# Performance work log

Hardware: AMD Instinct MI355X
Metric: run time of the kernel (lower is better)

## Reference

```python
import jax, jax.numpy as jnp
import numpy as np

BLANK_IDX = -1  # resolves to V-1
BATCH_FIRST = False
IS_PROBS = False


def setup_inputs() -> dict:
    key = jax.random.key(0)
    k1, k2 = jax.random.split(key)
    T, N, V = 2048, 32, 1024
    logits = jax.random.normal(k1, (T, N, V), dtype=jnp.float32)
    in_lens = jax.random.randint(k2, (N,), 1, T + 1).astype(jnp.int64)
    return {"logits": logits, "in_lens": in_lens}


def reference(logits, in_lens):
    # logits: (T, N, V) since batch_first=False
    V = logits.shape[2]
    blank = (BLANK_IDX + V) % V  # = V - 1
    logp = jax.nn.log_softmax(logits, axis=2)
    x = jnp.transpose(logp, (1, 0, 2))  # (N, T, V)
    max_ = jnp.max(x, axis=2)            # (N, T)
    argmax = jnp.argmax(x, axis=2)       # (N, T)
    N, T = argmax.shape

    keep = argmax != blank
    dedup = jnp.concatenate(
        [keep[:, :1], keep[:, 1:] & (argmax[:, 1:] != argmax[:, :-1])], axis=1
    )
    in_len_mask = jnp.arange(T)[None, :] < in_lens[:, None]  # (N, T)
    keep = dedup & in_len_mask
    max_ = jnp.where(in_len_mask, max_, 0.0)

    out_lens = keep.sum(axis=1)  # (N,)
    # stream compaction: position of each kept token within its row
    pos = jnp.cumsum(keep, axis=1) - 1               # (N, T)
    safe_pos = jnp.where(keep, pos, T)               # out-of-bounds -> dropped
    rows = jnp.broadcast_to(jnp.arange(N)[:, None], (N, T))
    # torch masked_scatter_ semantics: overwrite first out_lens[n] slots,
    # leave remaining entries as original argmax values ("undefined" region)
    paths = argmax.at[rows, safe_pos].set(argmax, mode="drop")

    max_total = max_.sum(axis=1)  # (N,)
    if not BATCH_FIRST:
        paths = paths.T  # (T, N)
    return max_total, paths, out_lens
```

## Files before the change

kernel.cpp:

```cpp
#include <hip/hip_runtime.h>
#include <hip/hip_bf16.h>


#define WAVE 64

template <int CH>
__global__ __launch_bounds__(256) void row_lse_kernel(
    const float* __restrict__ logits,
    float* __restrict__ rmaxT, int* __restrict__ rargT,
    int T, int N, int rows) {
  const int lane = threadIdx.x & (WAVE - 1);
  const int row  = blockIdx.x * (blockDim.x >> 6) + (threadIdx.x >> 6);
  if (row >= rows) return;
  const int V = CH * 256;
  const float* p = logits + (size_t)row * V;

  float m = -3.4e38f;
  int   mi = 0;
  float4 v[CH];
#pragma unroll
  for (int c = 0; c < CH; ++c) {
    const int idx = c * 256 + lane * 4;
    v[c] = *(const float4*)(p + idx);
    if (v[c].x > m) { m = v[c].x; mi = idx; }
    if (v[c].y > m) { m = v[c].y; mi = idx + 1; }
    if (v[c].z > m) { m = v[c].z; mi = idx + 2; }
    if (v[c].w > m) { m = v[c].w; mi = idx + 3; }
  }
#pragma unroll
  for (int off = 32; off; off >>= 1) {
    const float om = __shfl_down(m, off);
    const int   oi = __shfl_down(mi, off);
    if (om > m || (om == m && oi < mi)) { m = om; mi = oi; }
  }
  m = __shfl(m, 0);

  float s = 0.f;
#pragma unroll
  for (int c = 0; c < CH; ++c)
    s += __expf(v[c].x - m) + __expf(v[c].y - m) +
         __expf(v[c].z - m) + __expf(v[c].w - m);
#pragma unroll
  for (int off = 32; off; off >>= 1) s += __shfl_down(s, off);

  if (lane == 0) {
    const int t = row / N, n = row % N;
    rmaxT[(size_t)n * T + t] = -__logf(s);
    rargT[(size_t)n * T + t] = mi;
  }
}

__global__ __launch_bounds__(256) void row_lse_generic(
    const float* __restrict__ logits,
    float* __restrict__ rmaxT, int* __restrict__ rargT,
    int T, int N, int V, int rows) {
  const int lane = threadIdx.x & (WAVE - 1);
  const int row  = blockIdx.x * (blockDim.x >> 6) + (threadIdx.x >> 6);
  if (row >= rows) return;
  const float* p = logits + (size_t)row * V;

  float m = -3.4e38f; int mi = 0;
  for (int i = lane; i < V; i += WAVE) {
    const float x = p[i];
    if (x > m) { m = x; mi = i; }
  }
  for (int off = 32; off; off >>= 1) {
    const float om = __shfl_down(m, off);
    const int   oi = __shfl_down(mi, off);
    if (om > m || (om == m && oi < mi)) { m = om; mi = oi; }
  }
  m = __shfl(m, 0);
  float s = 0.f;
  for (int i = lane; i < V; i += WAVE) s += __expf(p[i] - m);
  for (int off = 32; off; off >>= 1) s += __shfl_down(s, off);
  if (lane == 0) {
    const int t = row / N, n = row % N;
    rmaxT[(size_t)n * T + t] = -__logf(s);
    rargT[(size_t)n * T + t] = mi;
  }
}

#define CB 256
__global__ __launch_bounds__(CB) void ctc_compact_kernel(
    const float* __restrict__ rmaxT, const int* __restrict__ rargT,
    const int* __restrict__ in_lens, float* __restrict__ out,
    int T, int N, int V) {
  const int n = blockIdx.x;
  const int tid = threadIdx.x;
  const int L = in_lens[n];
  const int blank = V - 1;
  const int items = (T + CB - 1) / CB;
  const int t0 = tid * items;

  float* out_total = out;
  float* out_paths = out + N;
  float* out_lens  = out + N + (size_t)T * N;

  const float* rm = rmaxT + (size_t)n * T;
  const int*   ra = rargT + (size_t)n * T;

  int   cnt = 0;
  float sum = 0.f;
  for (int i = 0; i < items; ++i) {
    const int t = t0 + i;
    if (t >= T) break;
    const int a = ra[t];
    bool keep = (t < L) && (a != blank);
    if (keep && t > 0) keep = (a != ra[t - 1]);
    cnt += keep ? 1 : 0;
    if (t < L) sum += rm[t];
    out_paths[(size_t)t * N + n] = (float)a;
  }

  __shared__ int   s_cnt[CB];
  __shared__ float s_sum[CB];
  s_cnt[tid] = cnt;
  s_sum[tid] = sum;
  __syncthreads();
  for (int off = 1; off < CB; off <<= 1) {
    const int   c  = (tid >= off) ? s_cnt[tid - off] : 0;
    const float sv = (tid >= off) ? s_sum[tid - off] : 0.f;
    __syncthreads();
    s_cnt[tid] += c;
    s_sum[tid] += sv;
    __syncthreads();
  }
  const int prefix = s_cnt[tid] - cnt;
  if (tid == 0) {
    out_total[n] = s_sum[CB - 1];
    out_lens[n]  = (float)s_cnt[CB - 1];
  }
  __syncthreads();

  int pos = prefix;
  for (int i = 0; i < items; ++i) {
    const int t = t0 + i;
    if (t >= T) break;
    const int a = ra[t];
    bool keep = (t < L) && (a != blank);
    if (keep && t > 0) keep = (a != ra[t - 1]);
    if (keep) {
      out_paths[(size_t)pos * N + n] = (float)a;
      ++pos;
    }
  }
}

extern "C" void kernel_launch(void* const* d_in, const int* in_sizes, int n_in,
                              void* d_out, int out_size, void* d_ws, size_t ws_size,
                              hipStream_t stream) {
  const float* logits = (const float*)d_in[0];
  const int* in_lens  = (const int*)d_in[1];
  float* out = (float*)d_out;

  const int N = in_sizes[1];
  const int T = (out_size - 2 * N) / N;
  const long long total = in_sizes[0];
  const int V = (int)(total / ((long long)T * N));
  const int rows = T * N;

  float* rmaxT = (float*)d_ws;
  int*   rargT = (int*)((char*)d_ws + (size_t)rows * sizeof(float));

  const int wavesPerBlock = 4;
  const int grid1 = (rows + wavesPerBlock - 1) / wavesPerBlock;

  if (V == 1024) {
    row_lse_kernel<4><<<grid1, 256, 0, stream>>>(logits, rmaxT, rargT, T, N, rows);
  } else if (V == 512) {
    row_lse_kernel<2><<<grid1, 256, 0, stream>>>(logits, rmaxT, rargT, T, N, rows);
  } else if (V == 2048) {
    row_lse_kernel<8><<<grid1, 256, 0, stream>>>(logits, rmaxT, rargT, T, N, rows);
  } else {
    row_lse_generic<<<grid1, 256, 0, stream>>>(logits, rmaxT, rargT, T, N, V, rows);
  }

  ctc_compact_kernel<<<N, CB, 0, stream>>>(rmaxT, rargT, in_lens, out, T, N, V);
}
```

Baseline: 359.4 us.

## Write raw argmax paths from LSE kernel, use nontemporal loads, carry prev argmax

The row-reduction kernel now writes the uncompacted argmax value for each (t,n) row directly into the output paths buffer, coalesced through shared memory. This removes the strided scatter of the full path array from the per-sequence compaction kernel, which now only overwrites the kept prefix. Logit loads become nontemporal to avoid polluting the cache on a streaming read. The compaction loops carry the previous argmax in a register instead of reloading it. One barrier is dropped, and the cross-kernel ordering between the two writes to the paths buffer is relied on for correctness.

```diff
diff --git a/kernel.cpp b/kernel.cpp
--- a/kernel.cpp
+++ b/kernel.cpp
@@ -3,25 +3,30 @@
 
 
 #define WAVE 64
+
+typedef float nvec4 __attribute__((ext_vector_type(4)));
 
 template <int CH>
 __global__ __launch_bounds__(256) void row_lse_kernel(
     const float* __restrict__ logits,
     float* __restrict__ rmaxT, int* __restrict__ rargT,
+    float* __restrict__ out_paths,
     int T, int N, int rows) {
   const int lane = threadIdx.x & (WAVE - 1);
-  const int row  = blockIdx.x * (blockDim.x >> 6) + (threadIdx.x >> 6);
-  if (row >= rows) return;
+  const int w    = threadIdx.x >> 6;
+  const int row  = blockIdx.x * 4 + w;
+  const bool active = row < rows;
   const int V = CH * 256;
-  const float* p = logits + (size_t)row * V;
+  const float* p = logits + (size_t)(active ? row : 0) * V;
+  const nvec4* p4 = (const nvec4*)p;
 
   float m = -3.4e38f;
   int   mi = 0;
-  float4 v[CH];
+  nvec4 v[CH];
 #pragma unroll
   for (int c = 0; c < CH; ++c) {
+    v[c] = __builtin_nontemporal_load(p4 + c * 64 + lane);
     const int idx = c * 256 + lane * 4;
-    v[c] = *(const float4*)(p + idx);
     if (v[c].x > m) { m = v[c].x; mi = idx; }
     if (v[c].y > m) { m = v[c].y; mi = idx + 1; }
     if (v[c].z > m) { m = v[c].z; mi = idx + 2; }
@@ -43,21 +48,30 @@
 #pragma unroll
   for (int off = 32; off; off >>= 1) s += __shfl_down(s, off);
 
-  if (lane == 0) {
+  __shared__ float s_path[4];
+  if (lane == 0 && active) {
     const int t = row / N, n = row % N;
     rmaxT[(size_t)n * T + t] = -__logf(s);
     rargT[(size_t)n * T + t] = mi;
+    s_path[w] = (float)mi;
+  }
+  __syncthreads();
+  if (threadIdx.x < 4) {
+    const int r = blockIdx.x * 4 + threadIdx.x;
+    if (r < rows) out_paths[r] = s_path[threadIdx.x];
   }
 }
 
 __global__ __launch_bounds__(256) void row_lse_generic(
     const float* __restrict__ logits,
     float* __restrict__ rmaxT, int* __restrict__ rargT,
+    float* __restrict__ out_paths,
     int T, int N, int V, int rows) {
   const int lane = threadIdx.x & (WAVE - 1);
-  const int row  = blockIdx.x * (blockDim.x >> 6) + (threadIdx.x >> 6);
-  if (row >= rows) return;
-  const float* p = logits + (size_t)row * V;
+  const int w    = threadIdx.x >> 6;
+  const int row  = blockIdx.x * 4 + w;
+  const bool active = row < rows;
+  const float* p = logits + (size_t)(active ? row : 0) * V;
 
   float m = -3.4e38f; int mi = 0;
   for (int i = lane; i < V; i += WAVE) {
@@ -73,10 +87,18 @@
   float s = 0.f;
   for (int i = lane; i < V; i += WAVE) s += __expf(p[i] - m);
   for (int off = 32; off; off >>= 1) s += __shfl_down(s, off);
-  if (lane == 0) {
+
+  __shared__ float s_path[4];
+  if (lane == 0 && active) {
     const int t = row / N, n = row % N;
     rmaxT[(size_t)n * T + t] = -__logf(s);
     rargT[(size_t)n * T + t] = mi;
+    s_path[w] = (float)mi;
+  }
+  __syncthreads();
+  if (threadIdx.x < 4) {
+    const int r = blockIdx.x * 4 + threadIdx.x;
+    if (r < rows) out_paths[r] = s_path[threadIdx.x];
   }
 }
 
@@ -101,15 +123,15 @@
 
   int   cnt = 0;
   float sum = 0.f;
+  int prev = (t0 > 0 && t0 <= T) ? ra[t0 - 1] : -1;
   for (int i = 0; i < items; ++i) {
     const int t = t0 + i;
     if (t >= T) break;
     const int a = ra[t];
-    bool keep = (t < L) && (a != blank);
-    if (keep && t > 0) keep = (a != ra[t - 1]);
+    const bool keep = (t < L) && (a != blank) && (t == 0 || a != prev);
+    prev = a;
     cnt += keep ? 1 : 0;
     if (t < L) sum += rm[t];
-    out_paths[(size_t)t * N + n] = (float)a;
   }
 
   __shared__ int   s_cnt[CB];
@@ -130,15 +152,15 @@
     out_total[n] = s_sum[CB - 1];
     out_lens[n]  = (float)s_cnt[CB - 1];
   }
-  __syncthreads();
 
   int pos = prefix;
+  prev = (t0 > 0 && t0 <= T) ? ra[t0 - 1] : -1;
   for (int i = 0; i < items; ++i) {
     const int t = t0 + i;
     if (t >= T) break;
     const int a = ra[t];
-    bool keep = (t < L) && (a != blank);
-    if (keep && t > 0) keep = (a != ra[t - 1]);
+    const bool keep = (t < L) && (a != blank) && (t == 0 || a != prev);
+    prev = a;
     if (keep) {
       out_paths[(size_t)pos * N + n] = (float)a;
       ++pos;
@@ -161,18 +183,18 @@
 
   float* rmaxT = (float*)d_ws;
   int*   rargT = (int*)((char*)d_ws + (size_t)rows * sizeof(float));
-
-  const int wavesPerBlock = 4;
-  const int grid1 = (rows + wavesPerBlock - 1) / wavesPerBlock;
+  float* out_paths = out + N;
+
+  const int grid1 = (rows + 3) / 4;
 
   if (V == 1024) {
-    row_lse_kernel<4><<<grid1, 256, 0, stream>>>(logits, rmaxT, rargT, T, N, rows);
+    row_lse_kernel<4><<<grid1, 256, 0, stream>>>(logits, rmaxT, rargT, out_paths, T, N, rows);
   } else if (V == 512) {
-    row_lse_kernel<2><<<grid1, 256, 0, stream>>>(logits, rmaxT, rargT, T, N, rows);
+    row_lse_kernel<2><<<grid1, 256, 0, stream>>>(logits, rmaxT, rargT, out_paths, T, N, rows);
   } else if (V == 2048) {
-    row_lse_kernel<8><<<grid1, 256, 0, stream>>>(logits, rmaxT, rargT, T, N, rows);
+    row_lse_kernel<8><<<grid1, 256, 0, stream>>>(logits, rmaxT, rargT, out_paths, T, N, rows);
   } else {
-    row_lse_generic<<<grid1, 256, 0, stream>>>(logits, rmaxT, rargT, T, N, V, rows);
+    row_lse_generic<<<grid1, 256, 0, stream>>>(logits, rmaxT, rargT, out_paths, T, N, V, rows);
   }
 
   ctc_compact_kernel<<<N, CB, 0, stream>>>(rmaxT, rargT, in_lens, out, T, N, V);
```

Result: faster. 335.1 us (-6.8%).
